# Kernel optimization log

Measured on AMD Instinct MI355X. Metric: run time of the kernel, lower is better.

## Reference

```python
import jax, jax.numpy as jnp
import numpy as np

B, S, D, H, FF = 4, 1024, 1024, 8, 4096
DK = D // H
EPS = 1e-5


def layernorm(x, g, b):
    m = jnp.mean(x, axis=-1, keepdims=True)
    v = jnp.mean(jnp.square(x - m), axis=-1, keepdims=True)
    return (x - m) * jax.lax.rsqrt(v + EPS) * g + b


def setup_inputs() -> dict:
    key = jax.random.key(0)
    ks = jax.random.split(key, 8)
    w = lambda k, shape: jax.random.normal(k, shape, jnp.float32) * 0.02
    return {
        "x": jax.random.normal(ks[0], (B, S, D), jnp.float32),
        "mask": jnp.ones((B, 1, 1, S), jnp.int32),  # unused in 'infer' mode, kept for fidelity
        "g1": jnp.ones((D,), jnp.float32), "b1": jnp.zeros((D,), jnp.float32),
        "Wq": w(ks[1], (D, D)), "bq": jnp.zeros((D,), jnp.float32),
        "Wk": w(ks[2], (D, D)), "bk": jnp.zeros((D,), jnp.float32),
        "Wv": w(ks[3], (D, H * D)), "bv": jnp.zeros((H * D,), jnp.float32),
        "g2": jnp.ones((D,), jnp.float32), "b2": jnp.zeros((D,), jnp.float32),
        "W1": w(ks[4], (D, FF)), "bw1": jnp.zeros((FF,), jnp.float32),
        "W2": w(ks[5], (FF, D)), "bw2": jnp.zeros((D,), jnp.float32),
    }


def reference(x, mask, g1, b1, Wq, bq, Wk, bk, Wv, bv, g2, b2, W1, bw1, W2, bw2):
    # --- MultiHeadedAttention (mode='infer'; mask is ignored by this path) ---
    xn = layernorm(x, g1, b1)                                   # [B,S,D]
    q = (xn @ Wq + bq).reshape(B, S, H, DK).transpose(0, 2, 1, 3)  # [B,H,S,DK]
    k = (xn @ Wk + bk).reshape(B, S, H, DK).transpose(0, 2, 1, 3)  # [B,H,S,DK]
    v = (xn @ Wv + bv).reshape(B, S, H, D).transpose(0, 2, 1, 3)   # [B,H,S,D]
    scores = jnp.einsum('bhqd,bhkd->bhqk', q, k) / jnp.sqrt(jnp.float32(DK))
    p = jax.nn.softmax(scores, axis=-1)                          # [B,H,S,S]
    ctx = jnp.einsum('bhqk,bhkd->bhqd', p, v)                    # [B,H,S,D]
    # Source does x.view(-1, B, dim, h).sum(heads).view(B, S, dim) on the
    # contiguous [B,H,S,D] tensor: a raw row-major reshape, reproduced exactly.
    attn_out = ctx.reshape(S, B, D, H).sum(axis=-1).reshape(B, S, D)
    # --- residual + SublayerConnection (pre-norm GELU FFN) ---
    x1 = x + attn_out
    xn2 = layernorm(x1, g2, b2)
    ffn = jax.nn.gelu(xn2 @ W1 + bw1, approximate=False) @ W2 + bw2
    return x1 + ffn
```

## Files before the change

kernel.cpp:

```cpp
#include <hip/hip_runtime.h>
#include <hip/hip_bf16.h>
#include <math.h>

typedef __attribute__((ext_vector_type(8))) short   short8;
typedef __attribute__((ext_vector_type(4))) short   short4v;
typedef __attribute__((ext_vector_type(8))) __bf16  bf16x8;
typedef __attribute__((ext_vector_type(4))) float   f32x4;

typedef const __attribute__((address_space(1))) void cgv_t;
typedef __attribute__((address_space(3))) void lv_t;

__device__ __forceinline__ float bs2f(short s) {
  unsigned int u = ((unsigned int)(unsigned short)s) << 16;
  return __builtin_bit_cast(float, u);
}
__device__ __forceinline__ short f2bs(float f) {
  __hip_bfloat16 h = __float2bfloat16(f);
  return __builtin_bit_cast(short, h);
}
__device__ __forceinline__ void glds16(const short* g, short* l) {
  __builtin_amdgcn_global_load_lds((cgv_t*)g, (lv_t*)l, 16, 0, 0);
}


__global__ __launch_bounds__(256) void transpose_k(const float* __restrict__ in,
                                                   short* __restrict__ out,
                                                   int R, int C) {
  __shared__ __align__(16) short T[64 * 72];
  const int r0 = blockIdx.y * 64, c0 = blockIdx.x * 64;
  const int t = threadIdx.x;
  {
    const int rr = t >> 4;
    const int cc = (t & 15) << 2;
#pragma unroll
    for (int h = 0; h < 4; h++) {
      const int row = rr + h * 16;
      f32x4 v = *(const f32x4*)(in + (long)(r0 + row) * C + c0 + cc);
#pragma unroll
      for (int e = 0; e < 4; e++) T[row * 72 + cc + e] = f2bs(v[e]);
    }
  }
  __syncthreads();
  {
    const int cr = t >> 3;
    const int rs = (t & 7) << 3;
#pragma unroll
    for (int h = 0; h < 2; h++) {
      const int c = cr + h * 32;
      short8 v;
#pragma unroll
      for (int e = 0; e < 8; e++) v[e] = T[(rs + e) * 72 + c];
      *(short8*)(out + (long)(c0 + c) * R + r0 + rs) = v;
    }
  }
}

__global__ __launch_bounds__(256) void tr16_k(const short* __restrict__ in,
                                              short* __restrict__ out) {
  __shared__ __align__(16) short T[64 * 72];
  const int c0 = blockIdx.x * 64;
  const int r0 = blockIdx.y * 64;
  const int t = threadIdx.x;
  {
    const int row = t >> 2, cs = (t & 3) << 4;
    short8 v0 = *(const short8*)(in + (long)(r0 + row) * 1024 + c0 + cs);
    short8 v1 = *(const short8*)(in + (long)(r0 + row) * 1024 + c0 + cs + 8);
    *(short8*)&T[row * 72 + cs] = v0;
    *(short8*)&T[row * 72 + cs + 8] = v1;
  }
  __syncthreads();
  const int bb = r0 >> 10, s0 = r0 & 1023;
  const int cr = t >> 3, rs = (t & 7) << 3;
#pragma unroll
  for (int half = 0; half < 2; half++) {
    const int c = cr + half * 32;
    const int gcol = c0 + c;
    const int head = gcol >> 7, g = gcol & 127;
    short8 v;
#pragma unroll
    for (int e = 0; e < 8; e++) v[e] = T[(rs + e) * 72 + c];
    *(short8*)(out + ((long)(bb * 8 + head)) * 131072 + (long)g * 1024 + s0 + rs) = v;
  }
}

__global__ __launch_bounds__(256) void wv8_k(const float* __restrict__ Wv,
                                             short* __restrict__ out) {
  __shared__ __align__(16) short T[64 * 72];
  const int r0 = blockIdx.x * 64, k0 = blockIdx.y * 64;
  const int t = threadIdx.x;
  const int wave = t >> 6, lane = t & 63;
  const int r = r0 + lane;
#pragma unroll 4
  for (int i = 0; i < 16; i++) {
    const int k = k0 + wave * 16 + i;
    const float* src = Wv + (long)k * 8192 + 8 * r;
    f32x4 a = *(const f32x4*)src;
    f32x4 b = *(const f32x4*)(src + 4);
    float s = (a[0] + a[1] + a[2] + a[3]) + (b[0] + b[1] + b[2] + b[3]);
    T[lane * 72 + wave * 16 + i] = f2bs(s);
  }
  __syncthreads();
  const int rr = t >> 3, kc = (t & 7) << 3;
#pragma unroll
  for (int half = 0; half < 2; half++) {
    const int rl = rr + half * 32;
    *(short8*)(out + (long)(r0 + rl) * 1024 + k0 + kc) = *(const short8*)&T[rl * 72 + kc];
  }
}

__global__ __launch_bounds__(256) void bv8_k(const float* __restrict__ bv,
                                             float* __restrict__ out) {
  const int r = blockIdx.x * 256 + threadIdx.x;
  f32x4 a = *(const f32x4*)(bv + 8 * r);
  f32x4 b = *(const f32x4*)(bv + 8 * r + 4);
  out[r] = (a[0] + a[1] + a[2] + a[3]) + (b[0] + b[1] + b[2] + b[3]);
}

__global__ __launch_bounds__(256) void ln_k(const float* __restrict__ in,
                                            const float* __restrict__ g,
                                            const float* __restrict__ b,
                                            short* __restrict__ out) {
  const int t = threadIdx.x;
  const long base = (long)blockIdx.x * 1024 + t * 4;
  f32x4 f = *(const f32x4*)(in + base);
  float v[4] = {f[0], f[1], f[2], f[3]};
  float s1 = v[0] + v[1] + v[2] + v[3];
  float s2 = v[0]*v[0] + v[1]*v[1] + v[2]*v[2] + v[3]*v[3];
#pragma unroll
  for (int off = 32; off; off >>= 1) {
    s1 += __shfl_xor(s1, off);
    s2 += __shfl_xor(s2, off);
  }
  __shared__ float rs[4], rq[4];
  if ((t & 63) == 0) { rs[t >> 6] = s1; rq[t >> 6] = s2; }
  __syncthreads();
  s1 = rs[0] + rs[1] + rs[2] + rs[3];
  s2 = rq[0] + rq[1] + rq[2] + rq[3];
  const float mean = s1 * (1.0f / 1024.0f);
  const float var  = s2 * (1.0f / 1024.0f) - mean * mean;
  const float rstd = rsqrtf(var + 1e-5f);
  f32x4 gv = *(const f32x4*)(g + t * 4);
  f32x4 bv = *(const f32x4*)(b + t * 4);
  short4v o;
#pragma unroll
  for (int i = 0; i < 4; i++)
    o[i] = f2bs((v[i] - mean) * rstd * gv[i] + bv[i]);
  *(short4v*)(out + base) = o;
}

__global__ __launch_bounds__(256) void reduce4_k(const float* __restrict__ p,
                                                 const float* __restrict__ x1,
                                                 const float* __restrict__ bias,
                                                 float* __restrict__ out) {
  const int t = threadIdx.x;
  const long base = (long)blockIdx.x * 1024 + t * 4;
  f32x4 a = *(const f32x4*)(p + base);
  f32x4 b = *(const f32x4*)(p + 4194304 + base);
  f32x4 c = *(const f32x4*)(p + 8388608 + base);
  f32x4 d = *(const f32x4*)(p + 12582912 + base);
  f32x4 e = *(const f32x4*)(x1 + base);
  f32x4 g = *(const f32x4*)(bias + t * 4);
  *(f32x4*)(out + base) = a + b + c + d + e + g;
}

__global__ __launch_bounds__(256, 2) void flash_k(
    const short* __restrict__ Qg_, const short* __restrict__ Kg_,
    const short* __restrict__ V8T, const float* __restrict__ xg,
    float* __restrict__ x1) {
  __shared__ __align__(16) short smem[40960];
  short* Qs = smem;
  short* Ks = smem + 8192;
  short* Vs = smem + 24576;

  const int t = threadIdx.x;
  const int wave = t >> 6, lane = t & 63;
  const int llo = lane & 15, lhi = lane >> 4;
  const int q0 = blockIdx.x * 64;
  const int bh = blockIdx.y, b = bh >> 3, h = bh & 7;

  const short* Qg = Qg_ + ((long)(b * 1024 + q0)) * 1024 + h * 128;
  const short* Kg = Kg_ + ((long)b * 1024) * 1024 + h * 128;
  const short* Vg = V8T + (long)bh * 131072;

  const int srow = t >> 2;
  const int sgc = (((t & 3) ^ ((t >> 3) & 3)) << 3);
  const int wbase = wave * 512;
  const int swzo = ((lhi ^ ((llo >> 1) & 3)) << 3);
  const int arow = (wave * 16 + llo) * 32 + swzo;

#pragma unroll
  for (int kk = 0; kk < 4; kk++)
    glds16(Qg + (long)srow * 1024 + kk * 32 + sgc, Qs + kk * 2048 + wbase);

  f32x4 o[8];
  float mR[4], lR[4];
#pragma unroll
  for (int i = 0; i < 8; i++) o[i] = f32x4{0.f, 0.f, 0.f, 0.f};
#pragma unroll
  for (int r = 0; r < 4; r++) { mR[r] = -1e30f; lR[r] = 0.f; }

  for (int it = 0; it < 8; it++) {
    const int kt0 = it * 128;
#pragma unroll
    for (int kk = 0; kk < 4; kk++) {
      glds16(Kg + (long)(kt0 + srow) * 1024 + kk * 32 + sgc,
             Ks + kk * 4096 + wbase);
      glds16(Kg + (long)(kt0 + 64 + srow) * 1024 + kk * 32 + sgc,
             Ks + kk * 4096 + 2048 + wbase);
      glds16(Vg + (long)srow * 1024 + kt0 + kk * 32 + sgc,
             Vs + kk * 4096 + wbase);
      glds16(Vg + (long)(64 + srow) * 1024 + kt0 + kk * 32 + sgc,
             Vs + kk * 4096 + 2048 + wbase);
    }
    __syncthreads();

    f32x4 s[8];
#pragma unroll
    for (int i = 0; i < 8; i++) s[i] = f32x4{0.f, 0.f, 0.f, 0.f};
#pragma unroll
    for (int kk = 0; kk < 4; kk++) {
      bf16x8 aq = *(const bf16x8*)(Qs + kk * 2048 + arow);
#pragma unroll
      for (int ct = 0; ct < 8; ct++) {
        bf16x8 bk = *(const bf16x8*)(Ks + kk * 4096 + (ct * 16 + llo) * 32 + swzo);
        s[ct] = __builtin_amdgcn_mfma_f32_16x16x32_bf16(aq, bk, s[ct], 0, 0, 0);
      }
    }
    float alpha[4];
#pragma unroll
    for (int r = 0; r < 4; r++) {
      float mt = s[0][r];
#pragma unroll
      for (int ct = 1; ct < 8; ct++) mt = fmaxf(mt, s[ct][r]);
      mt = fmaxf(mt, __shfl_xor(mt, 1));
      mt = fmaxf(mt, __shfl_xor(mt, 2));
      mt = fmaxf(mt, __shfl_xor(mt, 4));
      mt = fmaxf(mt, __shfl_xor(mt, 8));
      const float mn = fmaxf(mR[r], mt);
      alpha[r] = __builtin_amdgcn_exp2f(mR[r] - mn);
      mR[r] = mn;
    }
#pragma unroll
    for (int ct = 0; ct < 8; ct++)
#pragma unroll
      for (int r = 0; r < 4; r++)
        s[ct][r] = __builtin_amdgcn_exp2f(s[ct][r] - mR[r]);
#pragma unroll
    for (int ct = 0; ct < 8; ct++)
#pragma unroll
      for (int r = 0; r < 4; r++) o[ct][r] *= alpha[r];
#pragma unroll
    for (int r = 0; r < 4; r++) {
      float ls = s[0][r];
#pragma unroll
      for (int ct = 1; ct < 8; ct++) ls += s[ct][r];
      ls += __shfl_xor(ls, 1);
      ls += __shfl_xor(ls, 2);
      ls += __shfl_xor(ls, 4);
      ls += __shfl_xor(ls, 8);
      lR[r] = lR[r] * alpha[r] + ls;
    }
    __syncthreads();

#pragma unroll
    for (int ct = 0; ct < 8; ct++) {
      const int chunk = ((ct & 1) << 1) | (llo >> 3);
      const int cl = llo & 7;
#pragma unroll
      for (int r = 0; r < 4; r++) {
        const int row = wave * 16 + lhi * 4 + r;
        const int xr = ((lhi << 1) | (r >> 1)) & 3;
        Ks[(ct >> 1) * 4096 + row * 32 + (((chunk ^ xr) << 3) | cl)] = f2bs(s[ct][r]);
      }
    }
    __syncthreads();

#pragma unroll
    for (int kk = 0; kk < 4; kk++) {
      bf16x8 ap = *(const bf16x8*)(Ks + kk * 4096 + arow);
#pragma unroll
      for (int ct = 0; ct < 8; ct++) {
        bf16x8 bv = *(const bf16x8*)(Vs + kk * 4096 + (ct * 16 + llo) * 32 + swzo);
        o[ct] = __builtin_amdgcn_mfma_f32_16x16x32_bf16(ap, bv, o[ct], 0, 0, 0);
      }
    }
    __syncthreads();
  }

  float inv[4];
#pragma unroll
  for (int r = 0; r < 4; r++) inv[r] = 1.0f / lR[r];
#pragma unroll
  for (int ct = 0; ct < 8; ct++) {
#pragma unroll
    for (int r = 0; r < 4; r++) {
      const int row = q0 + wave * 16 + lhi * 4 + r;
      const long idx = ((long)(b * 8 + h) * 1024 + row) * 128 + ct * 16 + llo;
      x1[idx] = xg[idx] + o[ct][r] * inv[r];
    }
  }
}

enum { E_GELU = 0, E_QKV = 1, E_PART = 2 };

#define MF16(va, vb, vc) __builtin_amdgcn_mfma_f32_16x16x32_bf16(va, vb, vc, 0, 0, 0)
#define VMW(n) asm volatile("s_waitcnt vmcnt(" #n ")" ::: "memory")
#define NOPS ((void)0)

#define STAGE_A(BUF, KH, KB) do {                                          \
    glds16(Ag + (KB), smem + ((BUF) * 2 + (KH)) * 8192 + wofs);            \
    glds16(Ag2 + (KB), smem + ((BUF) * 2 + (KH)) * 8192 + 4096 + wofs);    \
  } while (0)
#define STAGE_B(BUF, KH, KB) do {                                          \
    glds16(Bg + (KB), smem + 32768 + ((BUF) * 2 + (KH)) * 8192 + wofs);    \
    glds16(Bg2 + (KB), smem + 32768 + ((BUF) * 2 + (KH)) * 8192 + 4096 + wofs); \
  } while (0)

#define PHASE(RH, KH, BUF, LOADB, STAGE_STMT, WAIT_STMT)                   \
  {                                                                        \
    const short* Ar_ = smem + ((BUF) * 2 + (KH)) * 8192 + aoff + (RH) * 2048; \
    bf16x8 a0 = *(const bf16x8*)(Ar_);                                     \
    bf16x8 a1 = *(const bf16x8*)(Ar_ + 512);                               \
    bf16x8 a2 = *(const bf16x8*)(Ar_ + 1024);                              \
    bf16x8 a3 = *(const bf16x8*)(Ar_ + 1536);                              \
    if (LOADB) {                                                           \
      const short* Br_ = smem + 32768 + ((BUF) * 2 + (KH)) * 8192 + boff;  \
      vb0 = *(const bf16x8*)(Br_);                                         \
      vb1 = *(const bf16x8*)(Br_ + 512);                                   \
      vb2 = *(const bf16x8*)(Br_ + 1024);                                  \
      vb3 = *(const bf16x8*)(Br_ + 1536);                                  \
    }                                                                      \
    STAGE_STMT;                                                            \
    __builtin_amdgcn_sched_barrier(0);                                     \
    __builtin_amdgcn_s_barrier();                                          \
    asm volatile("s_waitcnt lgkmcnt(0)" ::: "memory");                     \
    __builtin_amdgcn_sched_barrier(0);                                     \
    __builtin_amdgcn_s_setprio(1);                                         \
    acc[(RH) * 4 + 0][0] = MF16(a0, vb0, acc[(RH) * 4 + 0][0]);            \
    acc[(RH) * 4 + 0][1] = MF16(a0, vb1, acc[(RH) * 4 + 0][1]);            \
    acc[(RH) * 4 + 0][2] = MF16(a0, vb2, acc[(RH) * 4 + 0][2]);            \
    acc[(RH) * 4 + 0][3] = MF16(a0, vb3, acc[(RH) * 4 + 0][3]);            \
    acc[(RH) * 4 + 1][0] = MF16(a1, vb0, acc[(RH) * 4 + 1][0]);            \
    acc[(RH) * 4 + 1][1] = MF16(a1, vb1, acc[(RH) * 4 + 1][1]);            \
    acc[(RH) * 4 + 1][2] = MF16(a1, vb2, acc[(RH) * 4 + 1][2]);            \
    acc[(RH) * 4 + 1][3] = MF16(a1, vb3, acc[(RH) * 4 + 1][3]);            \
    acc[(RH) * 4 + 2][0] = MF16(a2, vb0, acc[(RH) * 4 + 2][0]);            \
    acc[(RH) * 4 + 2][1] = MF16(a2, vb1, acc[(RH) * 4 + 2][1]);            \
    acc[(RH) * 4 + 2][2] = MF16(a2, vb2, acc[(RH) * 4 + 2][2]);            \
    acc[(RH) * 4 + 2][3] = MF16(a2, vb3, acc[(RH) * 4 + 2][3]);            \
    acc[(RH) * 4 + 3][0] = MF16(a3, vb0, acc[(RH) * 4 + 3][0]);            \
    acc[(RH) * 4 + 3][1] = MF16(a3, vb1, acc[(RH) * 4 + 3][1]);            \
    acc[(RH) * 4 + 3][2] = MF16(a3, vb2, acc[(RH) * 4 + 3][2]);            \
    acc[(RH) * 4 + 3][3] = MF16(a3, vb3, acc[(RH) * 4 + 3][3]);            \
    __builtin_amdgcn_s_setprio(0);                                         \
    WAIT_STMT;                                                             \
    __builtin_amdgcn_sched_barrier(0);                                     \
    __builtin_amdgcn_s_barrier();                                          \
  }

#define TILE8(T, BUF)                                                        \
  PHASE(0, 0, BUF, 1, STAGE_A(1 - (BUF), 1, ((T) + 1) * 64 + 32), NOPS);     \
  PHASE(1, 0, BUF, 0, STAGE_B(1 - (BUF), 1, ((T) + 1) * 64 + 32), VMW(8));   \
  PHASE(0, 1, BUF, 1, STAGE_A(BUF, 0, ((T) + 2) * 64), NOPS);                \
  PHASE(1, 1, BUF, 0, STAGE_B(BUF, 0, ((T) + 2) * 64), VMW(8))

template <int EPI>
__global__ __launch_bounds__(512, 2) void gemm256(
    const short* __restrict__ A, int lda, long azk,
    const short* __restrict__ Bt, int ldb, long bzk,
    const float* __restrict__ bias, long biasl,
    void* __restrict__ outp, long czl, int ldc,
    void* __restrict__ aux, int K) {
  __shared__ __align__(16) short smem[65536];

  const int t = threadIdx.x;
  const int wave = t >> 6, lane = t & 63;
  const int llo = lane & 15, lhi = lane >> 4;
  const int wm = wave >> 2, wn = wave & 3;

  int lin = blockIdx.x + gridDim.x * (blockIdx.y + gridDim.y * blockIdx.z);
  const int nwg = gridDim.x * gridDim.y * gridDim.z;
  lin = (lin & 7) * (nwg >> 3) + (lin >> 3);
  const int bx = lin % gridDim.x;
  const int rem = lin / gridDim.x;
  const int by = rem % gridDim.y;
  const int z = rem / gridDim.y;

  const int bm0 = by * 256, bn0 = bx * 256;
  A += (long)z * azk;
  Bt += (long)z * bzk;

  const int srow = t >> 2;
  const int sgc = (((t & 3) ^ ((t >> 3) & 3)) << 3);
  const short* Ag  = A  + (long)(bm0 + srow) * lda + sgc;
  const short* Ag2 = A  + (long)(bm0 + 128 + srow) * lda + sgc;
  const short* Bg  = Bt + (long)(bn0 + srow) * ldb + sgc;
  const short* Bg2 = Bt + (long)(bn0 + 128 + srow) * ldb + sgc;
  const int wofs = wave * 512;

  const int swz = ((lhi ^ ((llo >> 1) & 3)) << 3);
  const int aoff = (wm * 128 + llo) * 32 + swz;
  const int boff = (wn * 64 + llo) * 32 + swz;

  f32x4 acc[8][4];
#pragma unroll
  for (int i = 0; i < 8; i++)
#pragma unroll
    for (int j = 0; j < 4; j++) acc[i][j] = f32x4{0.f, 0.f, 0.f, 0.f};
  bf16x8 vb0, vb1, vb2, vb3;

  const int NT = K >> 6;

  STAGE_A(0, 0, 0);  STAGE_B(0, 0, 0);
  STAGE_A(0, 1, 32); STAGE_B(0, 1, 32);
  STAGE_A(1, 0, 64); STAGE_B(1, 0, 64);
  VMW(8);
  __builtin_amdgcn_s_barrier();

  for (int tt = 0; tt < NT - 2; tt += 2) {
    TILE8(tt, 0);
    TILE8(tt + 1, 1);
  }
  PHASE(0, 0, 0, 1, STAGE_A(1, 1, (NT - 1) * 64 + 32), NOPS);
  PHASE(1, 0, 0, 0, STAGE_B(1, 1, (NT - 1) * 64 + 32), VMW(8));
  PHASE(0, 1, 0, 1, NOPS, NOPS);
  PHASE(1, 1, 0, 0, NOPS, VMW(4));
  PHASE(0, 0, 1, 1, NOPS, NOPS);
  PHASE(1, 0, 1, 0, NOPS, VMW(0));
  PHASE(0, 1, 1, 1, NOPS, NOPS);
  PHASE(1, 1, 1, 0, NOPS, NOPS);

  if (EPI == E_PART) {
    float* P = (float*)outp + (long)z * czl;
#pragma unroll
    for (int ct = 0; ct < 4; ct++) {
      const int col = bn0 + wn * 64 + ct * 16 + llo;
#pragma unroll
      for (int rt = 0; rt < 8; rt++) {
#pragma unroll
        for (int r = 0; r < 4; r++) {
          const int row = bm0 + wm * 128 + rt * 16 + lhi * 4 + r;
          P[(long)row * ldc + col] = acc[rt][ct][r];
        }
      }
    }
  } else {
    short* C = (short*)outp + (long)z * czl;
    if (EPI == E_QKV && z == 2) C = (short*)aux;
    short* slab = smem + wave * 4864;
    float bv4[4];
#pragma unroll
    for (int ct = 0; ct < 4; ct++)
      bv4[ct] = bias[z * biasl + bn0 + wn * 64 + ct * 16 + llo];
    const int rl0 = lane >> 3, cb8 = (lane & 7) << 3;
    const short* srd = slab + rl0 * 76 + cb8;
    short* Cw = C + (long)(bm0 + wm * 128 + rl0) * ldc + bn0 + wn * 64 + cb8;
#pragma unroll
    for (int p = 0; p < 2; p++) {
#pragma unroll
      for (int rt4 = 0; rt4 < 4; rt4++) {
#pragma unroll
        for (int ct = 0; ct < 4; ct++) {
#pragma unroll
          for (int r = 0; r < 4; r++) {
            float v = acc[p * 4 + rt4][ct][r] + bv4[ct];
            if (EPI == E_GELU)
              v = 0.5f * v * (1.0f + erff(v * 0.70710678118654752f));
            if (EPI == E_QKV && z == 0)
              v *= 0.12751744476582f;
            slab[(rt4 * 16 + lhi * 4 + r) * 76 + ct * 16 + llo] = f2bs(v);
          }
        }
      }
#pragma unroll
      for (int j = 0; j < 8; j++) {
        short8 v = *(const short8*)(srd + j * 8 * 76);
        *(short8*)(Cw + ((long)p * 64 + j * 8) * ldc) = v;
      }
    }
  }
}

extern "C" void kernel_launch(void* const* d_in, const int* in_sizes, int n_in,
                              void* d_out, int out_size, void* d_ws, size_t ws_size,
                              hipStream_t stream) {
  const float* x   = (const float*)d_in[0];
  const float* g1  = (const float*)d_in[2];
  const float* b1  = (const float*)d_in[3];
  const float* Wq  = (const float*)d_in[4];
  const float* bq  = (const float*)d_in[5];
  const float* Wk  = (const float*)d_in[6];
  const float* bk  = (const float*)d_in[7];
  const float* Wv  = (const float*)d_in[8];
  const float* bv  = (const float*)d_in[9];
  const float* g2  = (const float*)d_in[10];
  const float* b2  = (const float*)d_in[11];
  const float* W1  = (const float*)d_in[12];
  const float* bw1 = (const float*)d_in[13];
  const float* W2  = (const float*)d_in[14];
  const float* bw2 = (const float*)d_in[15];

  char* ws = (char*)d_ws;
  const long MB = 1024 * 1024;
  float* bQKV  = (float*)(ws);
  float* x1    = (float*)(ws + 1 * MB);
  short* wqT   = (short*)(ws + 17 * MB);
  short* wkT   = (short*)(ws + 19 * MB);
  short* wv8T  = (short*)(ws + 21 * MB);
  short* xn    = (short*)(ws + 23 * MB);
  short* Q     = (short*)(ws + 31 * MB);
  short* Kb    = (short*)(ws + 39 * MB);
  short* V8T   = (short*)(ws + 47 * MB);
  short* V8tmp = (short*)(ws + 55 * MB);
  short* xn2  = (short*)(ws + 17 * MB);
  short* Hb   = (short*)(ws + 25 * MB);
  short* w1T  = (short*)(ws + 57 * MB);
  short* w2T  = (short*)(ws + 65 * MB);
  float* part = (float*)(ws + 73 * MB);

  hipMemcpyAsync(bQKV, bq, 4096, hipMemcpyDeviceToDevice, stream);
  hipMemcpyAsync(bQKV + 1024, bk, 4096, hipMemcpyDeviceToDevice, stream);
  bv8_k<<<4, 256, 0, stream>>>(bv, bQKV + 2048);

  transpose_k<<<dim3(16, 16), 256, 0, stream>>>(Wq, wqT, 1024, 1024);
  transpose_k<<<dim3(16, 16), 256, 0, stream>>>(Wk, wkT, 1024, 1024);
  wv8_k<<<dim3(16, 16), 256, 0, stream>>>(Wv, wv8T);

  ln_k<<<4096, 256, 0, stream>>>(x, g1, b1, xn);

  gemm256<E_QKV><<<dim3(4, 16, 3), 512, 0, stream>>>(
      xn, 1024, 0, wqT, 1024, 1048576, bQKV, 1024,
      Q, 4194304, 1024, V8tmp, 1024);

  tr16_k<<<dim3(16, 64), 256, 0, stream>>>(V8tmp, V8T);

  flash_k<<<dim3(16, 32), 256, 0, stream>>>(Q, Kb, V8T, x, x1);

  transpose_k<<<dim3(64, 16), 256, 0, stream>>>(W1, w1T, 1024, 4096);
  transpose_k<<<dim3(16, 64), 256, 0, stream>>>(W2, w2T, 4096, 1024);

  ln_k<<<4096, 256, 0, stream>>>(x1, g2, b2, xn2);

  gemm256<E_GELU><<<dim3(16, 16, 1), 512, 0, stream>>>(
      xn2, 1024, 0, w1T, 1024, 0, bw1, 0,
      Hb, 0, 4096, nullptr, 1024);

  gemm256<E_PART><<<dim3(4, 16, 4), 512, 0, stream>>>(
      Hb, 4096, 1024, w2T, 4096, 1024, nullptr, 0,
      part, 4194304, 1024, nullptr, 1024);

  reduce4_k<<<4096, 256, 0, stream>>>(part, x1, bw2, (float*)d_out);
}
```

Baseline: 359.5 us.

## Fuse V transpose into QKV GEMM epilogue, lazy softmax rescale, remap flash blocks

The QKV GEMM now writes the V projection directly in transposed per-head layout through an LDS slab, which removes the separate tr16_k kernel and its intermediate buffer round-trip. In flash attention, the running max and rescale of the output and denominator are updated only when some row's new max exceeds the stored max by more than 8 (in log2 units). This skips the per-tile multiply of the output accumulators at the cost of a larger exp range in bf16/fp32. Flash block indices are also remapped so that neighbouring blocks spread across different heads and batches, which may change L2 reuse of K/V.

```diff
diff --git a/kernel.cpp b/kernel.cpp
--- a/kernel.cpp
+++ b/kernel.cpp
@@ -52,34 +52,6 @@
       for (int e = 0; e < 8; e++) v[e] = T[(rs + e) * 72 + c];
       *(short8*)(out + (long)(c0 + c) * R + r0 + rs) = v;
     }
-  }
-}
-
-__global__ __launch_bounds__(256) void tr16_k(const short* __restrict__ in,
-                                              short* __restrict__ out) {
-  __shared__ __align__(16) short T[64 * 72];
-  const int c0 = blockIdx.x * 64;
-  const int r0 = blockIdx.y * 64;
-  const int t = threadIdx.x;
-  {
-    const int row = t >> 2, cs = (t & 3) << 4;
-    short8 v0 = *(const short8*)(in + (long)(r0 + row) * 1024 + c0 + cs);
-    short8 v1 = *(const short8*)(in + (long)(r0 + row) * 1024 + c0 + cs + 8);
-    *(short8*)&T[row * 72 + cs] = v0;
-    *(short8*)&T[row * 72 + cs + 8] = v1;
-  }
-  __syncthreads();
-  const int bb = r0 >> 10, s0 = r0 & 1023;
-  const int cr = t >> 3, rs = (t & 7) << 3;
-#pragma unroll
-  for (int half = 0; half < 2; half++) {
-    const int c = cr + half * 32;
-    const int gcol = c0 + c;
-    const int head = gcol >> 7, g = gcol & 127;
-    short8 v;
-#pragma unroll
-    for (int e = 0; e < 8; e++) v[e] = T[(rs + e) * 72 + c];
-    *(short8*)(out + ((long)(bb * 8 + head)) * 131072 + (long)g * 1024 + s0 + rs) = v;
   }
 }
 
@@ -175,8 +147,11 @@
   const int t = threadIdx.x;
   const int wave = t >> 6, lane = t & 63;
   const int llo = lane & 15, lhi = lane >> 4;
-  const int q0 = blockIdx.x * 64;
-  const int bh = blockIdx.y, b = bh >> 3, h = bh & 7;
+
+  int lin = blockIdx.x + (blockIdx.y << 4);
+  lin = (lin & 7) * 64 + (lin >> 3);
+  const int q0 = (lin & 15) * 64;
+  const int bh = lin >> 4, b = bh >> 3, h = bh & 7;
 
   const short* Qg = Qg_ + ((long)(b * 1024 + q0)) * 1024 + h * 128;
   const short* Kg = Kg_ + ((long)b * 1024) * 1024 + h * 128;
@@ -226,29 +201,39 @@
         s[ct] = __builtin_amdgcn_mfma_f32_16x16x32_bf16(aq, bk, s[ct], 0, 0, 0);
       }
     }
-    float alpha[4];
+    float mt[4];
 #pragma unroll
     for (int r = 0; r < 4; r++) {
-      float mt = s[0][r];
-#pragma unroll
-      for (int ct = 1; ct < 8; ct++) mt = fmaxf(mt, s[ct][r]);
-      mt = fmaxf(mt, __shfl_xor(mt, 1));
-      mt = fmaxf(mt, __shfl_xor(mt, 2));
-      mt = fmaxf(mt, __shfl_xor(mt, 4));
-      mt = fmaxf(mt, __shfl_xor(mt, 8));
-      const float mn = fmaxf(mR[r], mt);
-      alpha[r] = __builtin_amdgcn_exp2f(mR[r] - mn);
-      mR[r] = mn;
+      float m = s[0][r];
+#pragma unroll
+      for (int ct = 1; ct < 8; ct++) m = fmaxf(m, s[ct][r]);
+      m = fmaxf(m, __shfl_xor(m, 1));
+      m = fmaxf(m, __shfl_xor(m, 2));
+      m = fmaxf(m, __shfl_xor(m, 4));
+      m = fmaxf(m, __shfl_xor(m, 8));
+      mt[r] = m;
+    }
+    bool need = (mt[0] > mR[0] + 8.f) | (mt[1] > mR[1] + 8.f) |
+                (mt[2] > mR[2] + 8.f) | (mt[3] > mR[3] + 8.f);
+    if (__any(need)) {
+      float alpha[4];
+#pragma unroll
+      for (int r = 0; r < 4; r++) {
+        const float mn = fmaxf(mR[r], mt[r]);
+        alpha[r] = __builtin_amdgcn_exp2f(mR[r] - mn);
+        mR[r] = mn;
+        lR[r] *= alpha[r];
+      }
+#pragma unroll
+      for (int ct = 0; ct < 8; ct++)
+#pragma unroll
+        for (int r = 0; r < 4; r++) o[ct][r] *= alpha[r];
     }
 #pragma unroll
     for (int ct = 0; ct < 8; ct++)
 #pragma unroll
       for (int r = 0; r < 4; r++)
         s[ct][r] = __builtin_amdgcn_exp2f(s[ct][r] - mR[r]);
-#pragma unroll
-    for (int ct = 0; ct < 8; ct++)
-#pragma unroll
-      for (int r = 0; r < 4; r++) o[ct][r] *= alpha[r];
 #pragma unroll
     for (int r = 0; r < 4; r++) {
       float ls = s[0][r];
@@ -258,7 +243,7 @@
       ls += __shfl_xor(ls, 2);
       ls += __shfl_xor(ls, 4);
       ls += __shfl_xor(ls, 8);
-      lR[r] = lR[r] * alpha[r] + ls;
+      lR[r] += ls;
     }
     __syncthreads();
 
@@ -444,9 +429,35 @@
         }
       }
     }
+  } else if (EPI == E_QKV && z == 2) {
+    short* slab = smem + wave * 4352;
+    const int bb = bm0 >> 10, sbase = (bm0 & 1023) + wm * 128;
+    float bv4[4];
+#pragma unroll
+    for (int ct = 0; ct < 4; ct++)
+      bv4[ct] = bias[z * biasl + bn0 + wn * 64 + ct * 16 + llo];
+    const int gcol = bn0 + wn * 64 + lane;
+    short* dst0 = (short*)aux + ((long)(bb * 8 + (gcol >> 7))) * 131072 +
+                  (long)(gcol & 127) * 1024 + sbase;
+#pragma unroll
+    for (int p = 0; p < 2; p++) {
+#pragma unroll
+      for (int rt4 = 0; rt4 < 4; rt4++) {
+#pragma unroll
+        for (int ct = 0; ct < 4; ct++) {
+#pragma unroll
+          for (int r = 0; r < 4; r++) {
+            float v = acc[p * 4 + rt4][ct][r] + bv4[ct];
+            slab[(ct * 16 + llo) * 68 + rt4 * 16 + lhi * 4 + r] = f2bs(v);
+          }
+        }
+      }
+#pragma unroll
+      for (int j = 0; j < 8; j++)
+        *(short8*)(dst0 + p * 64 + j * 8) = *(const short8*)&slab[lane * 68 + j * 8];
+    }
   } else {
     short* C = (short*)outp + (long)z * czl;
-    if (EPI == E_QKV && z == 2) C = (short*)aux;
     short* slab = smem + wave * 4864;
     float bv4[4];
 #pragma unroll
@@ -511,7 +522,6 @@
   short* Q     = (short*)(ws + 31 * MB);
   short* Kb    = (short*)(ws + 39 * MB);
   short* V8T   = (short*)(ws + 47 * MB);
-  short* V8tmp = (short*)(ws + 55 * MB);
   short* xn2  = (short*)(ws + 17 * MB);
   short* Hb   = (short*)(ws + 25 * MB);
   short* w1T  = (short*)(ws + 57 * MB);
@@ -530,9 +540,7 @@
 
   gemm256<E_QKV><<<dim3(4, 16, 3), 512, 0, stream>>>(
       xn, 1024, 0, wqT, 1024, 1048576, bQKV, 1024,
-      Q, 4194304, 1024, V8tmp, 1024);
-
-  tr16_k<<<dim3(16, 64), 256, 0, stream>>>(V8tmp, V8T);
+      Q, 4194304, 1024, V8T, 1024);
 
   flash_k<<<dim3(16, 32), 256, 0, stream>>>(Q, Kb, V8T, x, x1);
 
```

After: 355.2 us. Within noise of the previous version (-1.2%).
